# Kernel tuning notes

Hardware: AMD Instinct MI355X
Metric: run time of the kernel (lower is better)

The kernel has to match this reference:

```python
import jax, jax.numpy as jnp
import numpy as np

B_, C_, H_, W_, N_ = 2, 256, 64, 64, 16


def setup_inputs() -> dict:
    key = jax.random.key(0)
    ks = jax.random.split(key, 6)
    return {
        "features": jax.random.normal(ks[0], (B_, C_, H_, W_), jnp.float32),
        "A_log": jax.random.normal(ks[1], (C_, N_), jnp.float32) * 0.5,
        "D": jax.random.normal(ks[2], (C_,), jnp.float32),
        "W_delta": jax.random.normal(ks[3], (C_, C_), jnp.float32) * 0.02,
        "b_delta": jnp.zeros((C_,), jnp.float32),
        "W_B": jax.random.normal(ks[4], (C_, N_), jnp.float32) * 0.02,
        "W_C": jax.random.normal(ks[5], (C_, N_), jnp.float32) * 0.02,
    }


def _selective_scan(x, A_log, D, W_delta, b_delta, W_B, W_C):
    # x: (B, L, C) -> (B, L, C). Canonical S6 selective scan (mamba corrector).
    delta = jax.nn.softplus(x @ W_delta + b_delta)          # (B, L, C)
    Bm = x @ W_B                                            # (B, L, N)
    Cm = x @ W_C                                            # (B, L, N)
    A = -jnp.exp(A_log)                                     # (C, N), negative real
    dA = jnp.exp(delta[..., None] * A)                      # (B, L, C, N)
    dBx = (delta * x)[..., None] * Bm[:, :, None, :]        # (B, L, C, N)

    def combine(left, right):
        a_l, b_l = left
        a_r, b_r = right
        return (a_l * a_r, a_r * b_l + b_r)

    # h_t = dA_t * h_{t-1} + dBx_t, computed in parallel over L
    _, h = jax.lax.associative_scan(combine, (dA, dBx), axis=1)
    y = jnp.einsum('blcn,bln->blc', h, Cm) + x * D          # (B, L, C)
    return y


def reference(features, A_log, D, W_delta, b_delta, W_B, W_C):
    B, C, H, W = features.shape
    corr = lambda x: _selective_scan(x, A_log, D, W_delta, b_delta, W_B, W_C)

    # direction 1: row-major forward
    flat = features.reshape(B, C, H * W).transpose(0, 2, 1)        # (B, HW, C)
    out1 = corr(flat)
    # direction 2: row-major reversed
    out2 = jnp.flip(corr(jnp.flip(flat, axis=1)), axis=1)
    # direction 3: rows flipped vertically (flip over H), scan, flip back
    rows = features.transpose(0, 2, 3, 1)                          # (B, H, W, C)
    rows_f = jnp.flip(rows, axis=1).reshape(B, H * W, C)
    out3 = jnp.flip(corr(rows_f).reshape(B, H, W, C), axis=1).reshape(B, H * W, C)
    # direction 4: column-major, flipped over W, scan, flip + transpose back
    cols = features.transpose(0, 3, 2, 1)                          # (B, W, H, C)
    cols_f = jnp.flip(cols, axis=1).reshape(B, W * H, C)
    out4 = jnp.flip(corr(cols_f).reshape(B, W, H, C), axis=1)
    out4 = out4.transpose(0, 2, 1, 3).reshape(B, H * W, C)

    mamba_out = (out1 + out2 + out3 + out4) / 4                    # (B, HW, C)
    return mamba_out.transpose(0, 2, 1).reshape(B, C, H, W)
```

## Files before the change

### kernel.cpp

```cpp
#include <hip/hip_runtime.h>
#include <cstdint>
#include <cstddef>

#define BB 2
#define CC 256
#define NN 16
#define LL 4096
#define NCH 128
#define CLEN 32
#define LOG2E 1.4426950408889634f

typedef __attribute__((ext_vector_type(8))) short short8;
typedef __attribute__((ext_vector_type(4))) float f32x4;

__device__ __forceinline__ float softplus_f(float z) {
    return fmaxf(z, 0.f) + log1pf(expf(-fabsf(z)));
}

__device__ __forceinline__ uint32_t pack_bf2(float d, float u) {
    uint32_t lo = (__float_as_uint(d) + 0x8000u) >> 16;
    uint32_t hh = (__float_as_uint(u) + 0x8000u) & 0xffff0000u;
    return hh | lo;
}

__device__ __forceinline__ short bf16r(float f) {
    return (short)((__float_as_uint(f) + 0x8000u) >> 16);
}

__global__ __launch_bounds__(256) void k1_mfma(
    const float* __restrict__ feat, const float* __restrict__ Wd,
    const float* __restrict__ bd, const float* __restrict__ WB,
    const float* __restrict__ WC, uint32_t* __restrict__ du,
    float* __restrict__ Bm, float* __restrict__ Cm)
{
    int blk = blockIdx.x;
    int b  = blk >> 9;
    int lt = (blk >> 2) & 127;
    int ct = blk & 3;
    int l0 = lt * 32, c0 = ct * 64;
    const float* fbase = feat + (size_t)b * CC * LL;
    int lane = threadIdx.x & 63;
    int wq   = threadIdx.x >> 6;
    int m    = lane & 15;
    int quad = lane >> 4;
    int m0   = (wq & 1) * 16;
    int n0   = (wq >> 1) * 32;
    bool doBC = (ct == 0);
    const float* wBC = (wq >> 1) ? WC : WB;

    f32x4 acc0 = {0.f, 0.f, 0.f, 0.f};
    f32x4 acc1 = {0.f, 0.f, 0.f, 0.f};
    f32x4 accB = {0.f, 0.f, 0.f, 0.f};

    const float* aptr  = fbase + (size_t)(quad * 8) * LL + (l0 + m0 + m);
    const float* b0ptr = Wd    + (size_t)(quad * 8) * CC + (c0 + n0 + m);
    const float* b1ptr = b0ptr + 16;
    const float* bbptr = wBC   + (size_t)(quad * 8) * NN + m;

    for (int ks = 0; ks < 8; ++ks) {
        short8 af, bf0, bf1;
        #pragma unroll
        for (int j = 0; j < 8; ++j) {
            size_t kr = (size_t)(ks * 32 + j);
            af[j]  = bf16r(aptr [kr * LL]);
            bf0[j] = bf16r(b0ptr[kr * CC]);
            bf1[j] = bf16r(b1ptr[kr * CC]);
        }
        acc0 = __builtin_amdgcn_mfma_f32_16x16x32_bf16(af, bf0, acc0, 0, 0, 0);
        acc1 = __builtin_amdgcn_mfma_f32_16x16x32_bf16(af, bf1, acc1, 0, 0, 0);
        if (doBC) {
            short8 bbf;
            #pragma unroll
            for (int j = 0; j < 8; ++j)
                bbf[j] = bf16r(bbptr[(size_t)(ks * 32 + j) * NN]);
            accB = __builtin_amdgcn_mfma_f32_16x16x32_bf16(af, bbf, accB, 0, 0, 0);
        }
    }

    if (doBC) {
        float* dst = (wq >> 1) ? Cm : Bm;
        #pragma unroll
        for (int r = 0; r < 4; ++r) {
            int l = l0 + m0 + quad * 4 + r;
            dst[((size_t)b * LL + l) * NN + m] = accB[r];
        }
    }

    float bd0 = bd[c0 + n0 + m];
    float bd1 = bd[c0 + n0 + 16 + m];
    int cA = c0 + n0 + m;
    int cB = cA + 16;
    #pragma unroll
    for (int r = 0; r < 4; ++r) {
        int l = l0 + m0 + quad * 4 + r;
        float d0 = softplus_f(acc0[r] + bd0);
        float d1 = softplus_f(acc1[r] + bd1);
        float x0 = fbase[(size_t)cA * LL + l];
        float x1 = fbase[(size_t)cB * LL + l];
        du[((size_t)b * LL + l) * CC + cA] = pack_bf2(d0, d0 * x0);
        du[((size_t)b * LL + l) * CC + cB] = pack_bf2(d1, d1 * x1);
    }
}

__global__ __launch_bounds__(512) void p1_aggr(
    const uint32_t* __restrict__ du, const float* __restrict__ Bm,
    const float* __restrict__ A_log, float* __restrict__ P, float* __restrict__ S)
{
    int blk = blockIdx.x;
    int b  = (blk >> 7) & 1;
    int ch = blk & 127;
    int t = threadIdx.x;
    int c = t & 255;
    int nb = (t >> 8) * 8;
    __shared__ float sBm[CLEN * NN];
    __shared__ uint32_t sW[CLEN * 256];

    float A2[8];
    {
        const float4* al = (const float4*)(A_log + c * NN + nb);
        #pragma unroll
        for (int q = 0; q < 2; ++q) {
            float4 v = al[q];
            A2[q*4+0] = -expf(v.x) * LOG2E;
            A2[q*4+1] = -expf(v.y) * LOG2E;
            A2[q*4+2] = -expf(v.z) * LOG2E;
            A2[q*4+3] = -expf(v.w) * LOG2E;
        }
    }

    int p0, inner;
    if (blk < 256) { p0 = 32 * ch;                          inner = 1;  }
    else           { p0 = 63 - (ch >> 1) + 2048 * (ch & 1); inner = 64; }

    {
        int j = t >> 4, nn = t & 15;
        sBm[t] = Bm[((size_t)b * LL + (p0 + inner * j)) * NN + nn];
    }
    if (t < 256) {
        const uint32_t* dub = du + (size_t)b * LL * CC + c;
        uint32_t wt[CLEN];
        #pragma unroll
        for (int j = 0; j < CLEN; ++j) wt[j] = dub[(size_t)(p0 + inner * j) * CC];
        #pragma unroll
        for (int j = 0; j < CLEN; ++j) sW[j * 256 + c] = wt[j];
    }
    __syncthreads();

    if (blk < 256) {
        float Sf[8] = {}, Sr[8] = {}, pref[8];
        #pragma unroll
        for (int nn = 0; nn < 8; ++nn) pref[nn] = 1.f;
        float sumd = 0.f;
        #pragma unroll 1
        for (int j = 0; j < CLEN; ++j) {
            uint32_t wj = sW[j * 256 + c];
            float dx = __uint_as_float(wj << 16);
            float uy = __uint_as_float(wj & 0xffff0000u);
            sumd += dx;
            float dA[8];
            #pragma unroll
            for (int nn = 0; nn < 8; ++nn) dA[nn] = __builtin_amdgcn_exp2f(A2[nn] * dx);
            #pragma unroll
            for (int nn = 0; nn < 8; ++nn) {
                float Bu = uy * sBm[j * 16 + nb + nn];
                Sf[nn] = fmaf(dA[nn], Sf[nn], Bu);
                Sr[nn] = fmaf(pref[nn], Bu, Sr[nn]);
                pref[nn] *= dA[nn];
            }
        }
        size_t base0 = ((size_t)(b * 128 + ch)) * 4096 + (size_t)c * 16 + nb;
        size_t base1 = ((size_t)((2 + b) * 128 + (127 - ch))) * 4096 + (size_t)c * 16 + nb;
        #pragma unroll
        for (int nn = 0; nn < 8; ++nn) {
            P[base0 + nn] = __builtin_amdgcn_exp2f(A2[nn] * sumd);
            S[base0 + nn] = Sf[nn];
            S[base1 + nn] = Sr[nn];
        }
    } else {
        float Sv[8] = {};
        float sumd = 0.f;
        #pragma unroll 1
        for (int j = 0; j < CLEN; ++j) {
            uint32_t wj = sW[j * 256 + c];
            float dx = __uint_as_float(wj << 16);
            float uy = __uint_as_float(wj & 0xffff0000u);
            sumd += dx;
            float dA[8];
            #pragma unroll
            for (int nn = 0; nn < 8; ++nn) dA[nn] = __builtin_amdgcn_exp2f(A2[nn] * dx);
            #pragma unroll
            for (int nn = 0; nn < 8; ++nn)
                Sv[nn] = fmaf(dA[nn], Sv[nn], uy * sBm[j * 16 + nb + nn]);
        }
        size_t base = ((size_t)((4 + b) * 128 + ch)) * 4096 + (size_t)c * 16 + nb;
        #pragma unroll
        for (int nn = 0; nn < 8; ++nn) {
            P[base + nn] = __builtin_amdgcn_exp2f(A2[nn] * sumd);
            S[base + nn] = Sv[nn];
        }
    }
}

__global__ __launch_bounds__(128) void p2_scan(
    const float* __restrict__ P, const float* __restrict__ S, float* __restrict__ Hin)
{
    int r = blockIdx.x * 128 + threadIdx.x;
    int cn = r & 4095;
    int db = r >> 12;
    int d = db >> 1;
    int cls = (d == 1) ? 1 : ((d == 3) ? 2 : 0);
    int b = db & 1;
    const size_t sbase = ((size_t)(cls * 2 + b) * 128) * 4096 + cn;
    const size_t pbase = (d == 1) ? (((size_t)b * 128) * 4096 + cn) : sbase;
    const size_t obase = ((size_t)db * 128) * 4096 + cn;
    float h = 0.f;
    for (int g = 0; g < 16; ++g) {
        float pv[8], sv[8];
        #pragma unroll
        for (int i = 0; i < 8; ++i) {
            int ch = g * 8 + i;
            int chm = (d == 2) ? (126 - 2 * (ch >> 1) + (ch & 1)) : ch;
            int chp = (d == 1) ? (127 - ch) : chm;
            pv[i] = P[pbase + (size_t)chp * 4096];
            sv[i] = S[sbase + (size_t)chm * 4096];
        }
        #pragma unroll
        for (int i = 0; i < 8; ++i) {
            Hin[obase + (size_t)(g * 8 + i) * 4096] = h;
            h = fmaf(pv[i], h, sv[i]);
        }
    }
}

__global__ __launch_bounds__(256) void p3_replay(
    const uint32_t* __restrict__ du, const float* __restrict__ Bm,
    const float* __restrict__ Cm, const float* __restrict__ A_log,
    const float* __restrict__ Hin, float* __restrict__ yAB,
    float* __restrict__ yC)
{
    int blk = blockIdx.x;
    int b  = (blk >> 7) & 1;
    int ch = blk & 127;
    int c = threadIdx.x;
    __shared__ float sBm[CLEN * NN];
    __shared__ float sCm[CLEN * NN];
    __shared__ uint32_t sW[CLEN * 256];
    __shared__ float sY[CLEN * 256];

    float A2[NN];
    {
        const float4* al = (const float4*)(A_log + c * NN);
        #pragma unroll
        for (int q = 0; q < 4; ++q) {
            float4 v = al[q];
            A2[q*4+0] = -expf(v.x) * LOG2E;
            A2[q*4+1] = -expf(v.y) * LOG2E;
            A2[q*4+2] = -expf(v.z) * LOG2E;
            A2[q*4+3] = -expf(v.w) * LOG2E;
        }
    }

    if (blk < 256) {
        int p0 = 32 * ch;
        for (int i = threadIdx.x; i < CLEN * NN; i += 256) {
            int j = i >> 4, nn = i & 15;
            size_t o = ((size_t)b * LL + (p0 + j)) * NN + nn;
            sBm[i] = Bm[o];
            sCm[i] = Cm[o];
        }
        const uint32_t* dub = du + (size_t)b * LL * CC + c;
        {
            uint32_t wt[CLEN];
            #pragma unroll
            for (int j = 0; j < CLEN; ++j) wt[j] = dub[(size_t)(p0 + j) * CC];
            #pragma unroll
            for (int j = 0; j < CLEN; ++j) sW[j * 256 + c] = wt[j];
        }

        int chr = 127 - ch;
        float h1[NN];
        {
            const float4* hp1 = (const float4*)(Hin + ((size_t)(1 * 2 + b) * 128 + chr) * 4096 + (size_t)c * 16);
            #pragma unroll
            for (int q = 0; q < 4; ++q) {
                float4 v1 = hp1[q];
                h1[q*4+0]=v1.x; h1[q*4+1]=v1.y; h1[q*4+2]=v1.z; h1[q*4+3]=v1.w;
            }
        }
        __syncthreads();
        #pragma unroll 1
        for (int j = CLEN - 1; j >= 0; --j) {
            uint32_t wj = sW[j * 256 + c];
            float dx = __uint_as_float(wj << 16);
            float uy = __uint_as_float(wj & 0xffff0000u);
            float dA[NN];
            #pragma unroll
            for (int nn = 0; nn < NN; ++nn) dA[nn] = __builtin_amdgcn_exp2f(A2[nn] * dx);
            float yv = 0.f;
            #pragma unroll
            for (int nn = 0; nn < NN; ++nn) {
                float Bu = uy * sBm[j * 16 + nn];
                h1[nn] = fmaf(dA[nn], h1[nn], Bu);
                yv = fmaf(h1[nn], sCm[j * 16 + nn], yv);
            }
            sY[j * 256 + c] = yv;
        }

        int ch2 = 126 - (ch & ~1) + (ch & 1);
        float h0[NN], h2[NN];
        {
            const float4* hp0 = (const float4*)(Hin + ((size_t)(0 * 2 + b) * 128 + ch)  * 4096 + (size_t)c * 16);
            const float4* hp2 = (const float4*)(Hin + ((size_t)(2 * 2 + b) * 128 + ch2) * 4096 + (size_t)c * 16);
            #pragma unroll
            for (int q = 0; q < 4; ++q) {
                float4 v0 = hp0[q], v2 = hp2[q];
                h0[q*4+0]=v0.x; h0[q*4+1]=v0.y; h0[q*4+2]=v0.z; h0[q*4+3]=v0.w;
                h2[q*4+0]=v2.x; h2[q*4+1]=v2.y; h2[q*4+2]=v2.z; h2[q*4+3]=v2.w;
            }
        }
        #pragma unroll 1
        for (int j = 0; j < CLEN; ++j) {
            uint32_t wj = sW[j * 256 + c];
            float dx = __uint_as_float(wj << 16);
            float uy = __uint_as_float(wj & 0xffff0000u);
            float dA[NN];
            #pragma unroll
            for (int nn = 0; nn < NN; ++nn) dA[nn] = __builtin_amdgcn_exp2f(A2[nn] * dx);
            float y0v = 0.f, y2v = 0.f;
            #pragma unroll
            for (int nn = 0; nn < NN; ++nn) {
                float Bu = uy * sBm[j * 16 + nn];
                float cm = sCm[j * 16 + nn];
                h0[nn] = fmaf(dA[nn], h0[nn], Bu);
                h2[nn] = fmaf(dA[nn], h2[nn], Bu);
                y0v = fmaf(h0[nn], cm, y0v);
                y2v = fmaf(h2[nn], cm, y2v);
            }
            yAB[((size_t)b * LL + p0 + j) * CC + c] = 0.25f * (y0v + y2v + sY[j * 256 + c]);
        }
    } else {
        int p0 = 63 - (ch >> 1) + 2048 * (ch & 1);
        const int inner = 64;
        for (int i = threadIdx.x; i < CLEN * NN; i += 256) {
            int j = i >> 4, nn = i & 15;
            size_t o = ((size_t)b * LL + (p0 + inner * j)) * NN + nn;
            sBm[i] = Bm[o];
            sCm[i] = Cm[o];
        }
        const uint32_t* dub = du + (size_t)b * LL * CC + c;
        {
            uint32_t wt[CLEN];
            #pragma unroll
            for (int j = 0; j < CLEN; ++j) wt[j] = dub[(size_t)(p0 + inner * j) * CC];
            #pragma unroll
            for (int j = 0; j < CLEN; ++j) sW[j * 256 + c] = wt[j];
        }
        float h[NN];
        {
            const float4* hp = (const float4*)(Hin + ((size_t)(3 * 2 + b) * 128 + ch) * 4096 + (size_t)c * 16);
            #pragma unroll
            for (int q = 0; q < 4; ++q) {
                float4 v = hp[q];
                h[q*4+0]=v.x; h[q*4+1]=v.y; h[q*4+2]=v.z; h[q*4+3]=v.w;
            }
        }
        __syncthreads();
        #pragma unroll 1
        for (int j = 0; j < CLEN; ++j) {
            uint32_t wj = sW[j * 256 + c];
            float dx = __uint_as_float(wj << 16);
            float uy = __uint_as_float(wj & 0xffff0000u);
            float dA[NN];
            #pragma unroll
            for (int nn = 0; nn < NN; ++nn) dA[nn] = __builtin_amdgcn_exp2f(A2[nn] * dx);
            float yv = 0.f;
            #pragma unroll
            for (int nn = 0; nn < NN; ++nn) {
                float Bu = uy * sBm[j * 16 + nn];
                h[nn] = fmaf(dA[nn], h[nn], Bu);
                yv = fmaf(h[nn], sCm[j * 16 + nn], yv);
            }
            yC[((size_t)b * LL + p0 + inner * j) * CC + c] = 0.25f * yv;
        }
    }
}

__global__ __launch_bounds__(256) void k6_reduce(
    const float* __restrict__ feat, const float* __restrict__ D,
    const float* __restrict__ yAB, const float* __restrict__ yC,
    float* __restrict__ out)
{
    int pt = blockIdx.x & 63;
    int ct = (blockIdx.x >> 6) & 3;
    int b  = blockIdx.x >> 8;
    int p0 = pt * 64, c0 = ct * 64;
    __shared__ float tile[64 * 65];
    {
        int cl = threadIdx.x & 63;
        int pg = threadIdx.x >> 6;
        #pragma unroll
        for (int pp = 0; pp < 16; ++pp) {
            int pl = pp * 4 + pg;
            size_t ix = ((size_t)b * LL + p0 + pl) * CC + c0 + cl;
            tile[cl * 65 + pl] = yAB[ix] + yC[ix];
        }
    }
    __syncthreads();
    {
        int pl = threadIdx.x & 63;
        int cg = threadIdx.x >> 6;
        #pragma unroll
        for (int cc = 0; cc < 16; ++cc) {
            int cloc = cc * 4 + cg;
            int c = c0 + cloc;
            size_t o = ((size_t)b * CC + c) * LL + p0 + pl;
            out[o] = tile[cloc * 65 + pl] + feat[o] * D[c];
        }
    }
}

extern "C" void kernel_launch(void* const* d_in, const int* in_sizes, int n_in,
                              void* d_out, int out_size, void* d_ws, size_t ws_size,
                              hipStream_t stream)
{
    const float* feat  = (const float*)d_in[0];
    const float* A_log = (const float*)d_in[1];
    const float* D     = (const float*)d_in[2];
    const float* Wd    = (const float*)d_in[3];
    const float* bd    = (const float*)d_in[4];
    const float* WB    = (const float*)d_in[5];
    const float* WC    = (const float*)d_in[6];
    float* out = (float*)d_out;

    float* ws  = (float*)d_ws;
    uint32_t* du = (uint32_t*)ws;
    float* Bm  = ws  + (size_t)2097152;
    float* Cm  = Bm  + (size_t)131072;
    float* P   = Cm  + (size_t)131072;
    float* S   = P   + (size_t)3145728;
    float* Hin = S   + (size_t)3145728;
    float* yAB = Hin + (size_t)4194304;
    float* yC  = yAB + (size_t)2097152;

    k1_mfma<<<1024, 256, 0, stream>>>(feat, Wd, bd, WB, WC, du, Bm, Cm);
    p1_aggr<<<512, 512, 0, stream>>>(du, Bm, A_log, P, S);
    p2_scan<<<256, 128, 0, stream>>>(P, S, Hin);
    p3_replay<<<512, 256, 0, stream>>>(du, Bm, Cm, A_log, Hin, yAB, yC);
    k6_reduce<<<512, 256, 0, stream>>>(feat, D, yAB, yC, out);
}
```

Before: 151.2 us.

## Split p3 replay work across 512 threads by direction and state half

The replay kernel now runs 512 threads per block. For row chunks, one half runs the reverse-direction scan while the other half runs the two forward-style scans concurrently instead of sequentially. For column chunks, the 16 state dimensions are split between halves, and the partial outputs are combined through shared memory. The du tile load is also spread across all threads in p1 and p3. This adds shared memory (a second Y buffer) and an extra sync, and leaves the two halves unevenly loaded in the row case.

```diff
diff --git a/kernel.cpp b/kernel.cpp
--- a/kernel.cpp
+++ b/kernel.cpp
@@ -136,13 +136,15 @@
         int j = t >> 4, nn = t & 15;
         sBm[t] = Bm[((size_t)b * LL + (p0 + inner * j)) * NN + nn];
     }
-    if (t < 256) {
+    {
+        int jh = t >> 8;
         const uint32_t* dub = du + (size_t)b * LL * CC + c;
-        uint32_t wt[CLEN];
-        #pragma unroll
-        for (int j = 0; j < CLEN; ++j) wt[j] = dub[(size_t)(p0 + inner * j) * CC];
-        #pragma unroll
-        for (int j = 0; j < CLEN; ++j) sW[j * 256 + c] = wt[j];
+        uint32_t wt[16];
+        #pragma unroll
+        for (int jj = 0; jj < 16; ++jj)
+            wt[jj] = dub[(size_t)(p0 + inner * (jh * 16 + jj)) * CC];
+        #pragma unroll
+        for (int jj = 0; jj < 16; ++jj) sW[(jh * 16 + jj) * 256 + c] = wt[jj];
     }
     __syncthreads();
 
@@ -232,7 +234,7 @@
     }
 }
 
-__global__ __launch_bounds__(256) void p3_replay(
+__global__ __launch_bounds__(512) void p3_replay(
     const uint32_t* __restrict__ du, const float* __restrict__ Bm,
     const float* __restrict__ Cm, const float* __restrict__ A_log,
     const float* __restrict__ Hin, float* __restrict__ yAB,
@@ -241,146 +243,182 @@
     int blk = blockIdx.x;
     int b  = (blk >> 7) & 1;
     int ch = blk & 127;
-    int c = threadIdx.x;
+    int t = threadIdx.x;
+    int c = t & 255;
+    int half = t >> 8;
     __shared__ float sBm[CLEN * NN];
     __shared__ float sCm[CLEN * NN];
     __shared__ uint32_t sW[CLEN * 256];
     __shared__ float sY[CLEN * 256];
-
-    float A2[NN];
-    {
-        const float4* al = (const float4*)(A_log + c * NN);
-        #pragma unroll
-        for (int q = 0; q < 4; ++q) {
-            float4 v = al[q];
-            A2[q*4+0] = -expf(v.x) * LOG2E;
-            A2[q*4+1] = -expf(v.y) * LOG2E;
-            A2[q*4+2] = -expf(v.z) * LOG2E;
-            A2[q*4+3] = -expf(v.w) * LOG2E;
-        }
+    __shared__ float sY2[CLEN * 256];
+
+    int p0, inner;
+    if (blk < 256) { p0 = 32 * ch;                          inner = 1;  }
+    else           { p0 = 63 - (ch >> 1) + 2048 * (ch & 1); inner = 64; }
+
+    {
+        int j = t >> 4, nn = t & 15;
+        size_t o = ((size_t)b * LL + (p0 + inner * j)) * NN + nn;
+        sBm[t] = Bm[o];
+        sCm[t] = Cm[o];
+    }
+    {
+        int jh = half;
+        const uint32_t* dub = du + (size_t)b * LL * CC + c;
+        uint32_t wt[16];
+        #pragma unroll
+        for (int jj = 0; jj < 16; ++jj)
+            wt[jj] = dub[(size_t)(p0 + inner * (jh * 16 + jj)) * CC];
+        #pragma unroll
+        for (int jj = 0; jj < 16; ++jj) sW[(jh * 16 + jj) * 256 + c] = wt[jj];
     }
 
     if (blk < 256) {
-        int p0 = 32 * ch;
-        for (int i = threadIdx.x; i < CLEN * NN; i += 256) {
-            int j = i >> 4, nn = i & 15;
-            size_t o = ((size_t)b * LL + (p0 + j)) * NN + nn;
-            sBm[i] = Bm[o];
-            sCm[i] = Cm[o];
-        }
-        const uint32_t* dub = du + (size_t)b * LL * CC + c;
+        if (half) {
+            float A2[NN];
+            {
+                const float4* al = (const float4*)(A_log + c * NN);
+                #pragma unroll
+                for (int q = 0; q < 4; ++q) {
+                    float4 v = al[q];
+                    A2[q*4+0] = -expf(v.x) * LOG2E;
+                    A2[q*4+1] = -expf(v.y) * LOG2E;
+                    A2[q*4+2] = -expf(v.z) * LOG2E;
+                    A2[q*4+3] = -expf(v.w) * LOG2E;
+                }
+            }
+            int chr = 127 - ch;
+            float h1[NN];
+            {
+                const float4* hp1 = (const float4*)(Hin + ((size_t)(1 * 2 + b) * 128 + chr) * 4096 + (size_t)c * 16);
+                #pragma unroll
+                for (int q = 0; q < 4; ++q) {
+                    float4 v1 = hp1[q];
+                    h1[q*4+0]=v1.x; h1[q*4+1]=v1.y; h1[q*4+2]=v1.z; h1[q*4+3]=v1.w;
+                }
+            }
+            __syncthreads();
+            #pragma unroll 1
+            for (int j = CLEN - 1; j >= 0; --j) {
+                uint32_t wj = sW[j * 256 + c];
+                float dx = __uint_as_float(wj << 16);
+                float uy = __uint_as_float(wj & 0xffff0000u);
+                float dA[NN];
+                #pragma unroll
+                for (int nn = 0; nn < NN; ++nn) dA[nn] = __builtin_amdgcn_exp2f(A2[nn] * dx);
+                float yv = 0.f;
+                #pragma unroll
+                for (int nn = 0; nn < NN; ++nn) {
+                    float Bu = uy * sBm[j * 16 + nn];
+                    h1[nn] = fmaf(dA[nn], h1[nn], Bu);
+                    yv = fmaf(h1[nn], sCm[j * 16 + nn], yv);
+                }
+                sY[j * 256 + c] = yv;
+            }
+        } else {
+            float A2[NN];
+            {
+                const float4* al = (const float4*)(A_log + c * NN);
+                #pragma unroll
+                for (int q = 0; q < 4; ++q) {
+                    float4 v = al[q];
+                    A2[q*4+0] = -expf(v.x) * LOG2E;
+                    A2[q*4+1] = -expf(v.y) * LOG2E;
+                    A2[q*4+2] = -expf(v.z) * LOG2E;
+                    A2[q*4+3] = -expf(v.w) * LOG2E;
+                }
+            }
+            int ch2 = 126 - (ch & ~1) + (ch & 1);
+            float h0[NN], h2[NN];
+            {
+                const float4* hp0 = (const float4*)(Hin + ((size_t)(0 * 2 + b) * 128 + ch)  * 4096 + (size_t)c * 16);
+                const float4* hp2 = (const float4*)(Hin + ((size_t)(2 * 2 + b) * 128 + ch2) * 4096 + (size_t)c * 16);
+                #pragma unroll
+                for (int q = 0; q < 4; ++q) {
+                    float4 v0 = hp0[q], v2 = hp2[q];
+                    h0[q*4+0]=v0.x; h0[q*4+1]=v0.y; h0[q*4+2]=v0.z; h0[q*4+3]=v0.w;
+                    h2[q*4+0]=v2.x; h2[q*4+1]=v2.y; h2[q*4+2]=v2.z; h2[q*4+3]=v2.w;
+                }
+            }
+            __syncthreads();
+            #pragma unroll 1
+            for (int j = 0; j < CLEN; ++j) {
+                uint32_t wj = sW[j * 256 + c];
+                float dx = __uint_as_float(wj << 16);
+                float uy = __uint_as_float(wj & 0xffff0000u);
+                float dA[NN];
+                #pragma unroll
+                for (int nn = 0; nn < NN; ++nn) dA[nn] = __builtin_amdgcn_exp2f(A2[nn] * dx);
+                float y0v = 0.f, y2v = 0.f;
+                #pragma unroll
+                for (int nn = 0; nn < NN; ++nn) {
+                    float Bu = uy * sBm[j * 16 + nn];
+                    float cm = sCm[j * 16 + nn];
+                    h0[nn] = fmaf(dA[nn], h0[nn], Bu);
+                    h2[nn] = fmaf(dA[nn], h2[nn], Bu);
+                    y0v = fmaf(h0[nn], cm, y0v);
+                    y2v = fmaf(h2[nn], cm, y2v);
+                }
+                sY2[j * 256 + c] = y0v + y2v;
+            }
+        }
+        __syncthreads();
+        #pragma unroll
+        for (int k = 0; k < 16; ++k) {
+            int i = k * 512 + t;
+            int j = i >> 8, c2 = i & 255;
+            yAB[((size_t)b * LL + p0 + j) * CC + c2] =
+                0.25f * (sY[j * 256 + c2] + sY2[j * 256 + c2]);
+        }
+    } else {
+        int nb = half * 8;
+        float A2[8];
         {
-            uint32_t wt[CLEN];
-            #pragma unroll
-            for (int j = 0; j < CLEN; ++j) wt[j] = dub[(size_t)(p0 + j) * CC];
-            #pragma unroll
-            for (int j = 0; j < CLEN; ++j) sW[j * 256 + c] = wt[j];
-        }
-
-        int chr = 127 - ch;
-        float h1[NN];
+            const float4* al = (const float4*)(A_log + c * NN + nb);
+            #pragma unroll
+            for (int q = 0; q < 2; ++q) {
+                float4 v = al[q];
+                A2[q*4+0] = -expf(v.x) * LOG2E;
+                A2[q*4+1] = -expf(v.y) * LOG2E;
+                A2[q*4+2] = -expf(v.z) * LOG2E;
+                A2[q*4+3] = -expf(v.w) * LOG2E;
+            }
+        }
+        float h[8];
         {
-            const float4* hp1 = (const float4*)(Hin + ((size_t)(1 * 2 + b) * 128 + chr) * 4096 + (size_t)c * 16);
-            #pragma unroll
-            for (int q = 0; q < 4; ++q) {
-                float4 v1 = hp1[q];
-                h1[q*4+0]=v1.x; h1[q*4+1]=v1.y; h1[q*4+2]=v1.z; h1[q*4+3]=v1.w;
+            const float4* hp = (const float4*)(Hin + ((size_t)(3 * 2 + b) * 128 + ch) * 4096 + (size_t)c * 16 + nb);
+            #pragma unroll
+            for (int q = 0; q < 2; ++q) {
+                float4 v = hp[q];
+                h[q*4+0]=v.x; h[q*4+1]=v.y; h[q*4+2]=v.z; h[q*4+3]=v.w;
             }
         }
         __syncthreads();
-        #pragma unroll 1
-        for (int j = CLEN - 1; j >= 0; --j) {
-            uint32_t wj = sW[j * 256 + c];
-            float dx = __uint_as_float(wj << 16);
-            float uy = __uint_as_float(wj & 0xffff0000u);
-            float dA[NN];
-            #pragma unroll
-            for (int nn = 0; nn < NN; ++nn) dA[nn] = __builtin_amdgcn_exp2f(A2[nn] * dx);
-            float yv = 0.f;
-            #pragma unroll
-            for (int nn = 0; nn < NN; ++nn) {
-                float Bu = uy * sBm[j * 16 + nn];
-                h1[nn] = fmaf(dA[nn], h1[nn], Bu);
-                yv = fmaf(h1[nn], sCm[j * 16 + nn], yv);
-            }
-            sY[j * 256 + c] = yv;
-        }
-
-        int ch2 = 126 - (ch & ~1) + (ch & 1);
-        float h0[NN], h2[NN];
-        {
-            const float4* hp0 = (const float4*)(Hin + ((size_t)(0 * 2 + b) * 128 + ch)  * 4096 + (size_t)c * 16);
-            const float4* hp2 = (const float4*)(Hin + ((size_t)(2 * 2 + b) * 128 + ch2) * 4096 + (size_t)c * 16);
-            #pragma unroll
-            for (int q = 0; q < 4; ++q) {
-                float4 v0 = hp0[q], v2 = hp2[q];
-                h0[q*4+0]=v0.x; h0[q*4+1]=v0.y; h0[q*4+2]=v0.z; h0[q*4+3]=v0.w;
-                h2[q*4+0]=v2.x; h2[q*4+1]=v2.y; h2[q*4+2]=v2.z; h2[q*4+3]=v2.w;
-            }
-        }
+        float* dstp = half ? sY : sY2;
         #pragma unroll 1
         for (int j = 0; j < CLEN; ++j) {
             uint32_t wj = sW[j * 256 + c];
             float dx = __uint_as_float(wj << 16);
             float uy = __uint_as_float(wj & 0xffff0000u);
-            float dA[NN];
-            #pragma unroll
-            for (int nn = 0; nn < NN; ++nn) dA[nn] = __builtin_amdgcn_exp2f(A2[nn] * dx);
-            float y0v = 0.f, y2v = 0.f;
-            #pragma unroll
-            for (int nn = 0; nn < NN; ++nn) {
-                float Bu = uy * sBm[j * 16 + nn];
-                float cm = sCm[j * 16 + nn];
-                h0[nn] = fmaf(dA[nn], h0[nn], Bu);
-                h2[nn] = fmaf(dA[nn], h2[nn], Bu);
-                y0v = fmaf(h0[nn], cm, y0v);
-                y2v = fmaf(h2[nn], cm, y2v);
-            }
-            yAB[((size_t)b * LL + p0 + j) * CC + c] = 0.25f * (y0v + y2v + sY[j * 256 + c]);
-        }
-    } else {
-        int p0 = 63 - (ch >> 1) + 2048 * (ch & 1);
-        const int inner = 64;
-        for (int i = threadIdx.x; i < CLEN * NN; i += 256) {
-            int j = i >> 4, nn = i & 15;
-            size_t o = ((size_t)b * LL + (p0 + inner * j)) * NN + nn;
-            sBm[i] = Bm[o];
-            sCm[i] = Cm[o];
-        }
-        const uint32_t* dub = du + (size_t)b * LL * CC + c;
-        {
-            uint32_t wt[CLEN];
-            #pragma unroll
-            for (int j = 0; j < CLEN; ++j) wt[j] = dub[(size_t)(p0 + inner * j) * CC];
-            #pragma unroll
-            for (int j = 0; j < CLEN; ++j) sW[j * 256 + c] = wt[j];
-        }
-        float h[NN];
-        {
-            const float4* hp = (const float4*)(Hin + ((size_t)(3 * 2 + b) * 128 + ch) * 4096 + (size_t)c * 16);
-            #pragma unroll
-            for (int q = 0; q < 4; ++q) {
-                float4 v = hp[q];
-                h[q*4+0]=v.x; h[q*4+1]=v.y; h[q*4+2]=v.z; h[q*4+3]=v.w;
-            }
+            float dA[8];
+            #pragma unroll
+            for (int nn = 0; nn < 8; ++nn) dA[nn] = __builtin_amdgcn_exp2f(A2[nn] * dx);
+            float yv = 0.f;
+            #pragma unroll
+            for (int nn = 0; nn < 8; ++nn) {
+                float Bu = uy * sBm[j * 16 + nb + nn];
+                h[nn] = fmaf(dA[nn], h[nn], Bu);
+                yv = fmaf(h[nn], sCm[j * 16 + nb + nn], yv);
+            }
+            dstp[j * 256 + c] = yv;
         }
         __syncthreads();
-        #pragma unroll 1
-        for (int j = 0; j < CLEN; ++j) {
-            uint32_t wj = sW[j * 256 + c];
-            float dx = __uint_as_float(wj << 16);
-            float uy = __uint_as_float(wj & 0xffff0000u);
-            float dA[NN];
-            #pragma unroll
-            for (int nn = 0; nn < NN; ++nn) dA[nn] = __builtin_amdgcn_exp2f(A2[nn] * dx);
-            float yv = 0.f;
-            #pragma unroll
-            for (int nn = 0; nn < NN; ++nn) {
-                float Bu = uy * sBm[j * 16 + nn];
-                h[nn] = fmaf(dA[nn], h[nn], Bu);
-                yv = fmaf(h[nn], sCm[j * 16 + nn], yv);
-            }
-            yC[((size_t)b * LL + p0 + inner * j) * CC + c] = 0.25f * yv;
+        #pragma unroll
+        for (int k = 0; k < 16; ++k) {
+            int i = k * 512 + t;
+            int j = i >> 8, c2 = i & 255;
+            yC[((size_t)b * LL + p0 + inner * j) * CC + c2] =
+                0.25f * (sY[j * 256 + c2] + sY2[j * 256 + c2]);
         }
     }
 }
@@ -445,6 +483,6 @@
     k1_mfma<<<1024, 256, 0, stream>>>(feat, Wd, bd, WB, WC, du, Bm, Cm);
     p1_aggr<<<512, 512, 0, stream>>>(du, Bm, A_log, P, S);
     p2_scan<<<256, 128, 0, stream>>>(P, S, Hin);
-    p3_replay<<<512, 256, 0, stream>>>(du, Bm, Cm, A_log, Hin, yAB, yC);
+    p3_replay<<<512, 512, 0, stream>>>(du, Bm, Cm, A_log, Hin, yAB, yC);
     k6_reduce<<<512, 256, 0, stream>>>(feat, D, yAB, yC, out);
 }
```

Result: slower. 157.6 us (+4.2%).
